# Optimization experiments

Measured on AMD Instinct MI355X. Metric: run time of the kernel, lower is better.

The kernel has to match this reference:

```python
import jax, jax.numpy as jnp
import numpy as np

OUT, IN, GROUP = 11008, 4096, 64
NUM_GROUPS = IN // GROUP  # pad = 0 since IN % GROUP == 0


def setup_inputs() -> dict:
    key = jax.random.key(0)
    k_x, k_q, k_s, k_b = jax.random.split(key, 4)
    x = jax.random.normal(k_x, (4, 2048, IN), dtype=jnp.float32)
    # int4 symmetric codes in [-8, 7], stored as int8 like the torch buffer
    qweight = jax.random.randint(k_q, (OUT, NUM_GROUPS, GROUP), -8, 8).astype(jnp.int8)
    # positive per-group scales (amax/7 in the original), stored fp16
    scales = (jax.random.uniform(k_s, (OUT, NUM_GROUPS), dtype=jnp.float32) * 0.02 + 1e-3).astype(jnp.float16)
    bias = (jax.random.normal(k_b, (OUT,), dtype=jnp.float32) * 0.02).astype(jnp.float16)
    return {"x": x, "qweight": qweight, "scales": scales, "bias": bias}


def reference(x, qweight, scales, bias):
    # Fused dequant: w[o, g*GROUP + j] = q[o, g, j] * scales[o, g]
    w = (qweight.astype(jnp.float16) * scales[:, :, None]).reshape(OUT, IN)
    w = w.astype(x.dtype)  # original casts dequantized weight to x.dtype
    # F.linear(x, w, bias): y = x @ w.T + b  -> [B, S, OUT]
    return jnp.einsum('bsi,oi->bso', x, w) + bias.astype(x.dtype)
```

## Files before the change

kernel.cpp:

```cpp
#include <hip/hip_runtime.h>
#include <hip/hip_fp16.h>
#include <stdint.h>


#define M_DIM 8192
#define N_DIM 11008
#define K_DIM 4096
#define MT_TILES 32
#define NT_TILES 43
#define K_TILES 128
#define SLAB 8192

typedef short short8 __attribute__((ext_vector_type(8)));
typedef float floatx4 __attribute__((ext_vector_type(4)));

__device__ __forceinline__ unsigned short f2bf(float f) {
  union { float f; uint32_t u; } c; c.f = f;
  uint32_t u = c.u;
  return (unsigned short)((u + 0x7FFFu + ((u >> 16) & 1u)) >> 16);
}

__device__ __forceinline__ float load_sc(const void* p, size_t idx, bool is_f32) {
  if (is_f32) return ((const float*)p)[idx];
  return __half2float(((const __half*)p)[idx]);
}

__device__ __forceinline__ bool sniff_q_is_i32(const void* qv) {
  const int* w = (const int*)qv;
  bool ok = true;
  #pragma unroll
  for (int j = 0; j < 16; ++j) {
    int v = w[j];
    ok = ok && (v == (int)(signed char)(v & 0xFF));
  }
  return ok;
}
__device__ __forceinline__ bool sniff_s_is_f32(const void* sv) {
  const float* f = (const float*)sv;
  bool ok = true;
  #pragma unroll
  for (int j = 0; j < 8; ++j) {
    float v = f[j];
    ok = ok && (v > 4e-4f) && (v < 6e-2f);
  }
  return ok;
}

__device__ __forceinline__ void gload_lds16(const short* g, short* l) {
  __builtin_amdgcn_global_load_lds(
      (const __attribute__((address_space(1))) uint32_t*)g,
      (__attribute__((address_space(3))) uint32_t*)l, 16, 0, 0);
}

__global__ __launch_bounds__(256)
void cvt_x_pack(const float* __restrict__ x, short* __restrict__ xh) {
  const int b = blockIdx.x;
  const int mt = b >> 8;
  const int rem = b & 255;
  const int kt = rem >> 1, half = rem & 1;
  const int tid = threadIdx.x;
  const int r = half * 128 + (tid >> 1);
  const int s0 = (tid & 1) * 2;
  const int k0 = kt * 32 + s0 * 8;

  const float4* p = (const float4*)(x + (size_t)(mt * 256 + r) * K_DIM + k0);
  float4 f0 = p[0], f1 = p[1], f2 = p[2], f3 = p[3];
  short8 h0, h1;
  h0[0]=f2bf(f0.x); h0[1]=f2bf(f0.y); h0[2]=f2bf(f0.z); h0[3]=f2bf(f0.w);
  h0[4]=f2bf(f1.x); h0[5]=f2bf(f1.y); h0[6]=f2bf(f1.z); h0[7]=f2bf(f1.w);
  h1[0]=f2bf(f2.x); h1[1]=f2bf(f2.y); h1[2]=f2bf(f2.z); h1[3]=f2bf(f2.w);
  h1[4]=f2bf(f3.x); h1[5]=f2bf(f3.y); h1[6]=f2bf(f3.z); h1[7]=f2bf(f3.w);

  const int w = (r >> 1) & 3;
  short* slab = xh + ((size_t)mt * K_TILES + kt) * SLAB;
  *(short8*)&slab[r * 32 + ((s0    ) ^ w) * 8] = h0;
  *(short8*)&slab[r * 32 + ((s0 + 1) ^ w) * 8] = h1;
}

__global__ __launch_bounds__(256)
void deq_w_pack(const void* __restrict__ qv, const void* __restrict__ sv,
                short* __restrict__ wq) {
  const bool q_is_i32 = sniff_q_is_i32(qv);
  const bool s_is_f32 = sniff_s_is_f32(sv);
  const int b = blockIdx.x;
  const int nt = b >> 8;
  const int rem = b & 255;
  const int kt = rem >> 1, half = rem & 1;
  const int tid = threadIdx.x;
  const int r = half * 128 + (tid >> 1);
  const int s0 = (tid & 1) * 2;
  const int o = nt * 256 + r;
  const int k0 = kt * 32 + s0 * 8;

  const float s = load_sc(sv, (size_t)o * 64 + (kt >> 1), s_is_f32);

  int codes[16];
  if (q_is_i32) {
    const int* qq = (const int*)qv + (size_t)o * K_DIM + k0;
    #pragma unroll
    for (int j = 0; j < 4; ++j) {
      int4 t = ((const int4*)qq)[j];
      codes[j*4+0]=t.x; codes[j*4+1]=t.y; codes[j*4+2]=t.z; codes[j*4+3]=t.w;
    }
  } else {
    union { int4 v; int8_t c[16]; } u;
    u.v = *(const int4*)((const int8_t*)qv + (size_t)o * K_DIM + k0);
    #pragma unroll
    for (int j = 0; j < 16; ++j) codes[j] = (int)u.c[j];
  }

  short8 h0, h1;
  #pragma unroll
  for (int j = 0; j < 8; ++j) h0[j] = f2bf((float)codes[j] * s);
  #pragma unroll
  for (int j = 0; j < 8; ++j) h1[j] = f2bf((float)codes[8 + j] * s);

  const int w = (r >> 1) & 3;
  short* slab = wq + ((size_t)nt * K_TILES + kt) * SLAB;
  *(short8*)&slab[r * 32 + ((s0    ) ^ w) * 8] = h0;
  *(short8*)&slab[r * 32 + ((s0 + 1) ^ w) * 8] = h1;
}

__global__ __launch_bounds__(512, 2)
void gemm8(const short* __restrict__ xh, const short* __restrict__ wq,
           const void* __restrict__ sv, const void* __restrict__ bv,
           float* __restrict__ C) {
  __shared__ __align__(16) short lds[4 * 2 * SLAB];

  const bool s_is_f32 = sniff_s_is_f32(sv);

  const int tid  = threadIdx.x;
  const int lane = tid & 63;
  const int wid  = tid >> 6;
  const int wm = wid >> 2, wn = wid & 3;
  const int lr = lane & 15, lk = lane >> 4;

  const int bid = blockIdx.x;
  const int xcd = bid & 7;
  const int idx = bid >> 3;
  const int mt  = xcd * 4 + idx / NT_TILES;
  const int nt  = idx % NT_TILES;

  const short* Aslab = xh + (size_t)mt * K_TILES * SLAB;
  const short* Bslab = wq + (size_t)nt * K_TILES * SLAB;

  const int swz8 = (lk ^ ((lr >> 1) & 3)) << 3;
  int aoff[8], boff[4];
  #pragma unroll
  for (int mi = 0; mi < 8; ++mi) aoff[mi] = (wm * 128 + mi * 16 + lr) * 32 + swz8;
  #pragma unroll
  for (int ni = 0; ni < 4; ++ni) boff[ni] = (wn * 64 + ni * 16 + lr) * 32 + swz8;

  floatx4 acc[8][4];
  #pragma unroll
  for (int i = 0; i < 8; ++i)
    #pragma unroll
    for (int j = 0; j < 4; ++j)
      acc[i][j] = (floatx4){0.f, 0.f, 0.f, 0.f};

#define STAGE(t) do {                                                   \
    const short* ga_ = Aslab + (size_t)(t) * SLAB;                      \
    const short* gb_ = Bslab + (size_t)(t) * SLAB;                      \
    short* la_ = &lds[((t) & 3) * (2 * SLAB)];                          \
    short* lb_ = la_ + SLAB;                                            \
    gload_lds16(ga_ + tid * 8,        la_ + tid * 8);                   \
    gload_lds16(ga_ + 4096 + tid * 8, la_ + 4096 + tid * 8);            \
    gload_lds16(gb_ + tid * 8,        lb_ + tid * 8);                   \
    gload_lds16(gb_ + 4096 + tid * 8, lb_ + 4096 + tid * 8);            \
  } while (0)

#define COMPUTE(t) do {                                                 \
    const short* la_ = &lds[((t) & 3) * (2 * SLAB)];                    \
    const short* lb_ = la_ + SLAB;                                      \
    short8 a_[8], b_[4];                                                \
    _Pragma("unroll")                                                   \
    for (int mi = 0; mi < 8; ++mi) a_[mi] = *(const short8*)&la_[aoff[mi]]; \
    _Pragma("unroll")                                                   \
    for (int ni = 0; ni < 4; ++ni) b_[ni] = *(const short8*)&lb_[boff[ni]]; \
    __builtin_amdgcn_s_setprio(1);                                      \
    _Pragma("unroll")                                                   \
    for (int mi = 0; mi < 8; ++mi)                                      \
      _Pragma("unroll")                                                 \
      for (int ni = 0; ni < 4; ++ni)                                    \
        acc[mi][ni] = __builtin_amdgcn_mfma_f32_16x16x32_bf16(          \
            a_[mi], b_[ni], acc[mi][ni], 0, 0, 0);                      \
    __builtin_amdgcn_s_setprio(0);                                      \
  } while (0)

  STAGE(0); STAGE(1); STAGE(2);

  for (int kt = 0; kt < K_TILES - 3; ++kt) {
    STAGE(kt + 3);
    asm volatile("s_waitcnt vmcnt(12)" ::: "memory");
    __builtin_amdgcn_s_barrier();
    asm volatile("" ::: "memory");
    COMPUTE(kt);
    asm volatile("" ::: "memory");
    __builtin_amdgcn_s_barrier();
  }

  asm volatile("s_waitcnt vmcnt(8)" ::: "memory");
  __builtin_amdgcn_s_barrier();
  asm volatile("" ::: "memory");
  COMPUTE(K_TILES - 3);
  asm volatile("s_waitcnt vmcnt(4)" ::: "memory");
  __builtin_amdgcn_s_barrier();
  asm volatile("" ::: "memory");
  COMPUTE(K_TILES - 2);
  asm volatile("s_waitcnt vmcnt(0)" ::: "memory");
  __builtin_amdgcn_s_barrier();
  asm volatile("" ::: "memory");
  COMPUTE(K_TILES - 1);

#undef STAGE
#undef COMPUTE

  #pragma unroll
  for (int ni = 0; ni < 4; ++ni) {
    const int col = nt * 256 + wn * 64 + ni * 16 + lr;
    const float bvf = load_sc(bv, (size_t)col, s_is_f32);
    #pragma unroll
    for (int mi = 0; mi < 8; ++mi) {
      const int rbase = mt * 256 + wm * 128 + mi * 16 + lk * 4;
      #pragma unroll
      for (int rr = 0; rr < 4; ++rr)
        C[(size_t)(rbase + rr) * N_DIM + col] = acc[mi][ni][rr] + bvf;
    }
  }
}

__global__ __launch_bounds__(256)
void gemm_fused(const float* __restrict__ x, const void* __restrict__ qv,
                const void* __restrict__ sv, const void* __restrict__ bv,
                float* __restrict__ C) {
  __shared__ __align__(16) short As[128 * 64];
  __shared__ __align__(16) short Bs[128 * 64];

  const bool q_is_i32 = sniff_q_is_i32(qv);
  const bool s_is_f32 = sniff_s_is_f32(sv);

  const int tid  = threadIdx.x;
  const int lane = tid & 63;
  const int wid  = tid >> 6;
  const int wm = wid >> 1, wn = wid & 1;
  const int lr = lane & 15, lk = lane >> 4;

  const int nwg = gridDim.x;
  const int cpx = nwg >> 3;
  const int bid = blockIdx.x;
  const int swz = (bid & 7) * cpx + (bid >> 3);
  const int per_g = 4 * 86;
  const int g = swz / per_g;
  const int r = swz - g * per_g;
  const int mt = (g << 2) + (r & 3);
  const int nt = r >> 2;

  const int row0 = mt * 128;
  const int col0 = nt * 128;

  floatx4 acc[4][4];
  #pragma unroll
  for (int i = 0; i < 4; ++i)
    #pragma unroll
    for (int j = 0; j < 4; ++j)
      acc[i][j] = (floatx4){0.f, 0.f, 0.f, 0.f};

  for (int kt = 0; kt < K_DIM / 64; ++kt) {
    const int k0 = kt * 64;
    #pragma unroll
    for (int i = 0; i < 4; ++i) {
      const int cid = i * 256 + tid;
      const int arow = cid >> 3, ac = (cid & 7) << 3;
      const float4* p = (const float4*)(x + (size_t)(row0 + arow) * K_DIM + k0 + ac);
      float4 a = p[0], b = p[1];
      short8 h;
      h[0]=f2bf(a.x); h[1]=f2bf(a.y); h[2]=f2bf(a.z); h[3]=f2bf(a.w);
      h[4]=f2bf(b.x); h[5]=f2bf(b.y); h[6]=f2bf(b.z); h[7]=f2bf(b.w);
      *(short8*)&As[arow * 64 + ac] = h;
    }
    #pragma unroll
    for (int i = 0; i < 2; ++i) {
      const int cid = i * 256 + tid;
      const int brow = cid >> 2, bc = (cid & 3) << 4;
      const float s = load_sc(sv, (size_t)(col0 + brow) * 64 + kt, s_is_f32);
      int codes[16];
      if (q_is_i32) {
        const int* qq = (const int*)qv + (size_t)(col0 + brow) * K_DIM + k0 + bc;
        #pragma unroll
        for (int j = 0; j < 4; ++j) {
          int4 t = ((const int4*)qq)[j];
          codes[j*4+0]=t.x; codes[j*4+1]=t.y; codes[j*4+2]=t.z; codes[j*4+3]=t.w;
        }
      } else {
        union { int4 v; int8_t c[16]; } u;
        u.v = *(const int4*)((const int8_t*)qv + (size_t)(col0 + brow) * K_DIM + k0 + bc);
        #pragma unroll
        for (int j = 0; j < 16; ++j) codes[j] = (int)u.c[j];
      }
      short8 h0, h1;
      #pragma unroll
      for (int j = 0; j < 8; ++j) h0[j] = f2bf((float)codes[j] * s);
      #pragma unroll
      for (int j = 0; j < 8; ++j) h1[j] = f2bf((float)codes[8 + j] * s);
      *(short8*)&Bs[brow * 64 + bc]     = h0;
      *(short8*)&Bs[brow * 64 + bc + 8] = h1;
    }
    __syncthreads();
    #pragma unroll
    for (int ks = 0; ks < 2; ++ks) {
      short8 a[4], b[4];
      #pragma unroll
      for (int mi = 0; mi < 4; ++mi)
        a[mi] = *(const short8*)&As[(wm * 64 + mi * 16 + lr) * 64 + ks * 32 + lk * 8];
      #pragma unroll
      for (int ni = 0; ni < 4; ++ni)
        b[ni] = *(const short8*)&Bs[(wn * 64 + ni * 16 + lr) * 64 + ks * 32 + lk * 8];
      #pragma unroll
      for (int mi = 0; mi < 4; ++mi)
        #pragma unroll
        for (int ni = 0; ni < 4; ++ni)
          acc[mi][ni] = __builtin_amdgcn_mfma_f32_16x16x32_bf16(
              a[mi], b[ni], acc[mi][ni], 0, 0, 0);
    }
    __syncthreads();
  }

  #pragma unroll
  for (int ni = 0; ni < 4; ++ni) {
    const int col = col0 + wn * 64 + ni * 16 + lr;
    const float bvf = load_sc(bv, (size_t)col, s_is_f32);
    #pragma unroll
    for (int mi = 0; mi < 4; ++mi) {
      const int rbase = row0 + wm * 64 + mi * 16 + lk * 4;
      #pragma unroll
      for (int rr = 0; rr < 4; ++rr)
        C[(size_t)(rbase + rr) * N_DIM + col] = acc[mi][ni][rr] + bvf;
    }
  }
}

extern "C" void kernel_launch(void* const* d_in, const int* in_sizes, int n_in,
                              void* d_out, int out_size, void* d_ws, size_t ws_size,
                              hipStream_t stream) {
  const float* x  = (const float*)d_in[0];
  const void*  q  = (const void*)d_in[1];
  const void*  sc = (const void*)d_in[2];
  const void*  bs = (const void*)d_in[3];
  float* y = (float*)d_out;
  (void)in_sizes; (void)n_in; (void)out_size;

  const size_t xh_bytes = (size_t)M_DIM * K_DIM * 2;
  const size_t wq_bytes = (size_t)N_DIM * K_DIM * 2;

  if (ws_size >= xh_bytes + wq_bytes) {
    short* xh = (short*)d_ws;
    short* wq = (short*)((char*)d_ws + xh_bytes);
    cvt_x_pack<<<MT_TILES * 256, dim3(256), 0, stream>>>(x, xh);
    deq_w_pack<<<NT_TILES * 256, dim3(256), 0, stream>>>(q, sc, wq);
    gemm8<<<MT_TILES * NT_TILES * 8 / 8, dim3(512), 0, stream>>>(xh, wq, sc, bs, y);
  } else {
    gemm_fused<<<(M_DIM / 128) * (N_DIM / 128), dim3(256), 0, stream>>>(x, q, sc, bs, y);
  }
}
```

Baseline: 800.0 us.

## Double-buffer LDS fragments in registers and reorder tile mapping for reuse

Restructures the GEMM main loop so LDS-to-register fragment loads for the next k-tile run while MFMAs consume the current fragments (two register fragment sets, loop unrolled by two), with one barrier per tile instead of two. It also changes the block-to-tile mapping so consecutive blocks on an XCD share the same weight n-tile, improving L2 reuse of B. The occupancy hint of 2 blocks per CU is dropped from launch bounds, allowing more registers per thread at the cost of possibly lower occupancy.

After: 761.8 us. 4.8% less time.

```diff
diff --git a/kernel.cpp b/kernel.cpp
--- a/kernel.cpp
+++ b/kernel.cpp
@@ -121,7 +121,7 @@
   *(short8*)&slab[r * 32 + ((s0 + 1) ^ w) * 8] = h1;
 }
 
-__global__ __launch_bounds__(512, 2)
+__global__ __launch_bounds__(512)
 void gemm8(const short* __restrict__ xh, const short* __restrict__ wq,
            const void* __restrict__ sv, const void* __restrict__ bv,
            float* __restrict__ C) {
@@ -137,9 +137,9 @@
 
   const int bid = blockIdx.x;
   const int xcd = bid & 7;
-  const int idx = bid >> 3;
-  const int mt  = xcd * 4 + idx / NT_TILES;
-  const int nt  = idx % NT_TILES;
+  const int seq = bid >> 3;
+  const int nt  = seq >> 2;
+  const int mt  = xcd * 4 + (seq & 3);
 
   const short* Aslab = xh + (size_t)mt * K_TILES * SLAB;
   const short* Bslab = wq + (size_t)nt * K_TILES * SLAB;
@@ -158,62 +158,82 @@
     for (int j = 0; j < 4; ++j)
       acc[i][j] = (floatx4){0.f, 0.f, 0.f, 0.f};
 
+  short8 fa[8], fb[4], ga[8], gb[4];
+
 #define STAGE(t) do {                                                   \
-    const short* ga_ = Aslab + (size_t)(t) * SLAB;                      \
-    const short* gb_ = Bslab + (size_t)(t) * SLAB;                      \
-    short* la_ = &lds[((t) & 3) * (2 * SLAB)];                          \
-    short* lb_ = la_ + SLAB;                                            \
-    gload_lds16(ga_ + tid * 8,        la_ + tid * 8);                   \
-    gload_lds16(ga_ + 4096 + tid * 8, la_ + 4096 + tid * 8);            \
-    gload_lds16(gb_ + tid * 8,        lb_ + tid * 8);                   \
-    gload_lds16(gb_ + 4096 + tid * 8, lb_ + 4096 + tid * 8);            \
+    const short* gA_ = Aslab + (size_t)(t) * SLAB;                      \
+    const short* gB_ = Bslab + (size_t)(t) * SLAB;                      \
+    short* lA_ = &lds[((t) & 3) * (2 * SLAB)];                          \
+    short* lB_ = lA_ + SLAB;                                            \
+    gload_lds16(gA_ + tid * 8,        lA_ + tid * 8);                   \
+    gload_lds16(gA_ + 4096 + tid * 8, lA_ + 4096 + tid * 8);            \
+    gload_lds16(gB_ + tid * 8,        lB_ + tid * 8);                   \
+    gload_lds16(gB_ + 4096 + tid * 8, lB_ + 4096 + tid * 8);            \
   } while (0)
 
-#define COMPUTE(t) do {                                                 \
-    const short* la_ = &lds[((t) & 3) * (2 * SLAB)];                    \
-    const short* lb_ = la_ + SLAB;                                      \
-    short8 a_[8], b_[4];                                                \
+#define LOADF(da, db, t) do {                                           \
+    const short* lA_ = &lds[((t) & 3) * (2 * SLAB)];                    \
+    const short* lB_ = lA_ + SLAB;                                      \
     _Pragma("unroll")                                                   \
-    for (int mi = 0; mi < 8; ++mi) a_[mi] = *(const short8*)&la_[aoff[mi]]; \
+    for (int mi = 0; mi < 8; ++mi) da[mi] = *(const short8*)&lA_[aoff[mi]]; \
     _Pragma("unroll")                                                   \
-    for (int ni = 0; ni < 4; ++ni) b_[ni] = *(const short8*)&lb_[boff[ni]]; \
+    for (int ni = 0; ni < 4; ++ni) db[ni] = *(const short8*)&lB_[boff[ni]]; \
+  } while (0)
+
+#define DOMFMA(sa, sb) do {                                             \
     __builtin_amdgcn_s_setprio(1);                                      \
     _Pragma("unroll")                                                   \
     for (int mi = 0; mi < 8; ++mi)                                      \
       _Pragma("unroll")                                                 \
       for (int ni = 0; ni < 4; ++ni)                                    \
         acc[mi][ni] = __builtin_amdgcn_mfma_f32_16x16x32_bf16(          \
-            a_[mi], b_[ni], acc[mi][ni], 0, 0, 0);                      \
+            sa[mi], sb[ni], acc[mi][ni], 0, 0, 0);                      \
     __builtin_amdgcn_s_setprio(0);                                      \
   } while (0)
 
+#define FENCE asm volatile("" ::: "memory")
+#define VMCNT(n) asm volatile("s_waitcnt vmcnt(" #n ")" ::: "memory")
+#define BARRIER do { FENCE; __builtin_amdgcn_s_barrier(); FENCE; } while (0)
+
   STAGE(0); STAGE(1); STAGE(2);
-
-  for (int kt = 0; kt < K_TILES - 3; ++kt) {
+  VMCNT(8);
+  BARRIER;
+  LOADF(fa, fb, 0);
+
+  for (int kt = 0; kt < 124; kt += 2) {
+    VMCNT(4);
+    BARRIER;
     STAGE(kt + 3);
-    asm volatile("s_waitcnt vmcnt(12)" ::: "memory");
-    __builtin_amdgcn_s_barrier();
-    asm volatile("" ::: "memory");
-    COMPUTE(kt);
-    asm volatile("" ::: "memory");
-    __builtin_amdgcn_s_barrier();
-  }
-
-  asm volatile("s_waitcnt vmcnt(8)" ::: "memory");
-  __builtin_amdgcn_s_barrier();
-  asm volatile("" ::: "memory");
-  COMPUTE(K_TILES - 3);
-  asm volatile("s_waitcnt vmcnt(4)" ::: "memory");
-  __builtin_amdgcn_s_barrier();
-  asm volatile("" ::: "memory");
-  COMPUTE(K_TILES - 2);
-  asm volatile("s_waitcnt vmcnt(0)" ::: "memory");
-  __builtin_amdgcn_s_barrier();
-  asm volatile("" ::: "memory");
-  COMPUTE(K_TILES - 1);
+    LOADF(ga, gb, kt + 1);
+    DOMFMA(fa, fb);
+    VMCNT(4);
+    BARRIER;
+    STAGE(kt + 4);
+    LOADF(fa, fb, kt + 2);
+    DOMFMA(ga, gb);
+  }
+
+  VMCNT(4);
+  BARRIER;
+  STAGE(127);
+  LOADF(ga, gb, 125);
+  DOMFMA(fa, fb);
+  VMCNT(4);
+  BARRIER;
+  LOADF(fa, fb, 126);
+  DOMFMA(ga, gb);
+  VMCNT(0);
+  BARRIER;
+  LOADF(ga, gb, 127);
+  DOMFMA(fa, fb);
+  DOMFMA(ga, gb);
 
 #undef STAGE
-#undef COMPUTE
+#undef LOADF
+#undef DOMFMA
+#undef FENCE
+#undef VMCNT
+#undef BARRIER
 
   #pragma unroll
   for (int ni = 0; ni < 4; ++ni) {
@@ -357,7 +377,7 @@
     short* wq = (short*)((char*)d_ws + xh_bytes);
     cvt_x_pack<<<MT_TILES * 256, dim3(256), 0, stream>>>(x, xh);
     deq_w_pack<<<NT_TILES * 256, dim3(256), 0, stream>>>(q, sc, wq);
-    gemm8<<<MT_TILES * NT_TILES * 8 / 8, dim3(512), 0, stream>>>(xh, wq, sc, bs, y);
+    gemm8<<<MT_TILES * NT_TILES, dim3(512), 0, stream>>>(xh, wq, sc, bs, y);
   } else {
     gemm_fused<<<(M_DIM / 128) * (N_DIM / 128), dim3(256), 0, stream>>>(x, q, sc, bs, y);
   }
```
